# Optimization experiments

Measured on AMD Instinct MI355X. Metric: run time of the kernel, lower is better.

Reference implementation:

```python
import jax, jax.numpy as jnp
import numpy as np

N = 100000   # nodes
E = 1600000  # edges
D = 64       # hidden dim == num_features
L = 3        # num_gc_layers
C = 10       # num_classes
G = 512      # num graphs in batch
BN_EPS = 1e-5


def setup_inputs() -> dict:
    key = jax.random.key(0)
    ks = jax.random.split(key, 12)
    s = 1.0 / np.sqrt(D)
    return {
        "x": jax.random.normal(ks[0], (N, D), dtype=jnp.float32),
        "edge_index": jax.random.randint(ks[1], (2, E), 0, N, dtype=jnp.int64),
        "batch": jnp.sort(jax.random.randint(ks[2], (N,), 0, G, dtype=jnp.int64)),
        # GINConv MLP params (layer 0 input dim == D, so all layers stack)
        "w1": jax.random.normal(ks[3], (L, D, D), dtype=jnp.float32) * s,
        "b1": jnp.zeros((L, D), dtype=jnp.float32),
        "w2": jax.random.normal(ks[4], (L, D, D), dtype=jnp.float32) * s,
        "b2": jnp.zeros((L, D), dtype=jnp.float32),
        # BatchNorm affine params
        "gamma": jnp.ones((L, D), dtype=jnp.float32),
        "beta": jnp.zeros((L, D), dtype=jnp.float32),
        # final MLP
        "lin_w": jax.random.normal(ks[5], (L * D, D), dtype=jnp.float32) / np.sqrt(L * D),
        "lin_b": jnp.zeros((D,), dtype=jnp.float32),
        "fin_w": jax.random.normal(ks[6], (D, C), dtype=jnp.float32) * s,
        "fin_b": jnp.zeros((C,), dtype=jnp.float32),
    }


def reference(x, edge_index, batch, w1, b1, w2, b2, gamma, beta, lin_w, lin_b, fin_w, fin_b):
    src, dst = edge_index[0], edge_index[1]
    pooled = []
    h = x
    for i in range(L):
        # GINConv (eps=0): (1+eps)*h_i + sum_{j->i} h_j, then 2-layer MLP
        agg = h + jax.ops.segment_sum(h[src], dst, num_segments=N)  # [N, D]
        z = jax.nn.relu(agg @ w1[i] + b1[i]) @ w2[i] + b2[i]
        z = jax.nn.relu(z)
        # BatchNorm1d (training-mode batch statistics, biased variance)
        mean = jnp.mean(z, axis=0)
        var = jnp.var(z, axis=0)
        h = (z - mean) * (gamma[i] / jnp.sqrt(var + BN_EPS)) + beta[i]
        # global_add_pool: segment-sum over graph ids
        pooled.append(jax.ops.segment_sum(h, batch, num_segments=G))  # [G, D]
    xp = jnp.concatenate(pooled, axis=1)  # [G, L*D]
    out = jax.nn.relu(xp @ lin_w + lin_b) @ fin_w + fin_b  # [G, C]
    return jax.nn.log_softmax(out, axis=-1)
```

## Files before the change

### kernel.cpp

```cpp
#include <hip/hip_runtime.h>

#define BN_EPS 1e-5f
#define TN 128
#define NPB 256
#define BCAP 8192
#define BH_EPB 8192
#define PT_EPB 4096

typedef __attribute__((ext_vector_type(8))) short bf16x8;
typedef __attribute__((ext_vector_type(4))) float f32x4;

static __device__ __forceinline__ unsigned short f2bf(float f) {
    unsigned u = __float_as_uint(f);
    u += 0x7fff + ((u >> 16) & 1);
    return (unsigned short)(u >> 16);
}
static __device__ __forceinline__ float bf2f(unsigned short s) {
    return __uint_as_float(((unsigned)s) << 16);
}

__global__ __launch_bounds__(256) void xbf_kernel(
    const float* __restrict__ x, unsigned short* __restrict__ xbf, int n4)
{
    const int i = blockIdx.x * 256 + threadIdx.x;
    if (i < n4) {
        const float4 v = reinterpret_cast<const float4*>(x)[i];
        ushort4 o;
        o.x = f2bf(v.x); o.y = f2bf(v.y); o.z = f2bf(v.z); o.w = f2bf(v.w);
        reinterpret_cast<ushort4*>(xbf)[i] = o;
    }
}

__global__ __launch_bounds__(256) void bh_kernel(
    const int* __restrict__ dst, int* __restrict__ bucketCnt, int E, int NB)
{
    __shared__ int lh[512];
    const int tid = threadIdx.x;
    for (int i = tid; i < NB; i += 256) lh[i] = 0;
    __syncthreads();
    const int base = blockIdx.x * BH_EPB;
#pragma unroll
    for (int k = 0; k < BH_EPB / 256; ++k) {
        const int e = base + k * 256 + tid;
        if (e < E) atomicAdd(&lh[dst[e] >> 8], 1);
    }
    __syncthreads();
    for (int i = tid; i < NB; i += 256) {
        const int c = lh[i];
        if (c > 0) atomicAdd(&bucketCnt[i], c);
    }
}

__global__ __launch_bounds__(512) void bscan_kernel(
    const int* __restrict__ bucketCnt, int* __restrict__ bucketStart,
    int* __restrict__ bucketCursor, int NB)
{
    __shared__ int ls[512];
    const int t = threadIdx.x;
    const int v = (t < NB) ? bucketCnt[t] : 0;
    ls[t] = v;
    __syncthreads();
    for (int off = 1; off < 512; off <<= 1) {
        const int a = ls[t];
        const int b = (t >= off) ? ls[t - off] : 0;
        __syncthreads();
        ls[t] = a + b;
        __syncthreads();
    }
    const int excl = ls[t] - v;
    if (t < NB) { bucketStart[t] = excl; bucketCursor[t] = excl; }
    if (t == 511) bucketStart[NB] = ls[511];
}

__global__ __launch_bounds__(256) void part_kernel(
    const int* __restrict__ src, const int* __restrict__ dst,
    int* __restrict__ bucketCursor, unsigned* __restrict__ part, int E, int NB)
{
    __shared__ int lh[512];
    __shared__ int lbase[512];
    const int tid = threadIdx.x;
    const int base = blockIdx.x * PT_EPB;
    for (int i = tid; i < NB; i += 256) lh[i] = 0;
    __syncthreads();
#pragma unroll
    for (int k = 0; k < PT_EPB / 256; ++k) {
        const int e = base + k * 256 + tid;
        if (e < E) atomicAdd(&lh[dst[e] >> 8], 1);
    }
    __syncthreads();
    for (int i = tid; i < NB; i += 256) {
        const int c = lh[i];
        lbase[i] = (c > 0) ? atomicAdd(&bucketCursor[i], c) : 0;
        lh[i] = 0;
    }
    __syncthreads();
#pragma unroll
    for (int k = 0; k < PT_EPB / 256; ++k) {
        const int e = base + k * 256 + tid;
        if (e < E) {
            const int d = dst[e];
            const int b = d >> 8;
            const int off = atomicAdd(&lh[b], 1);
            part[lbase[b] + off] = ((unsigned)src[e] << 8) | (unsigned)(d & 255);
        }
    }
}

__global__ __launch_bounds__(256) void bcsr_kernel(
    const unsigned* __restrict__ part, const int* __restrict__ bucketStart,
    int* __restrict__ deg, int* __restrict__ rowstart,
    int* __restrict__ eidx, int nN)
{
    __shared__ unsigned sSrc[BCAP];
    __shared__ int ldeg[256], ls[256], lcur[256];
    const int b = blockIdx.x;
    const int tid = threadIdx.x;
    const int sStart = bucketStart[b];
    const int cnt = bucketStart[b + 1] - sStart;
    const bool ldsok = (cnt <= BCAP);

    ldeg[tid] = 0;
    __syncthreads();
    for (int i = tid; i < cnt; i += 256) {
        const unsigned v = part[sStart + i];
        if (ldsok) sSrc[i] = v;
        atomicAdd(&ldeg[v & 255u], 1);
    }
    __syncthreads();
    const int dv = ldeg[tid];
    ls[tid] = dv;
    __syncthreads();
    for (int off = 1; off < 256; off <<= 1) {
        const int a = ls[tid];
        const int c = (tid >= off) ? ls[tid - off] : 0;
        __syncthreads();
        ls[tid] = a + c;
        __syncthreads();
    }
    const int excl = ls[tid] - dv;
    lcur[tid] = excl;
    const int node = b * NPB + tid;
    if (node < nN) {
        deg[node] = dv;
        rowstart[node] = sStart + excl;
    }
    __syncthreads();
    for (int i = tid; i < cnt; i += 256) {
        const unsigned v = ldsok ? sSrc[i] : part[sStart + i];
        const int dloc = (int)(v & 255u);
        const int p = atomicAdd(&lcur[dloc], 1);
        eidx[sStart + p] = (int)(v >> 8);
    }
}

__global__ __launch_bounds__(256) void cnt_kernel(
    const int* __restrict__ batch, int* __restrict__ cnt, int nN)
{
    const int n = blockIdx.x * 256 + threadIdx.x;
    if (n >= nN) return;
    const int g = batch[n];
    const bool firstb = (n == 0) || (batch[n - 1] != g);
    const bool lastb  = (n == nN - 1) || (batch[n + 1] != g);
    if (lastb)  atomicAdd(&cnt[g], n + 1);
    if (firstb) atomicAdd(&cnt[g], -n);
}

__global__ __launch_bounds__(256) void agg_kernel(
    const unsigned short* __restrict__ z, const float* __restrict__ scsh,
    const int* __restrict__ rowstart, const int* __restrict__ deg,
    const int* __restrict__ eidx, unsigned short* __restrict__ agg, int nN)
{
    const int node = blockIdx.x * 4 + (threadIdx.x >> 6);
    if (node >= nN) return;
    const int lane = threadIdx.x & 63;
    const int q = lane >> 4;
    const int fr = (lane & 15) * 4;
    const int rs = rowstart[node];
    const int d = deg[node];

    float a0 = 0.f, a1 = 0.f, a2 = 0.f, a3 = 0.f;
    if (q == 0) {
        const ushort4 v = *reinterpret_cast<const ushort4*>(z + (size_t)node * 64 + fr);
        a0 = bf2f(v.x); a1 = bf2f(v.y); a2 = bf2f(v.z); a3 = bf2f(v.w);
    }
    for (int i = 0; i < d; i += 16) {
        const int j0 = i + q, j1 = j0 + 4, j2 = j0 + 8, j3 = j0 + 12;
        const int c0 = min(j0, d - 1), c1 = min(j1, d - 1);
        const int c2 = min(j2, d - 1), c3 = min(j3, d - 1);
        const int s0 = eidx[rs + c0], s1 = eidx[rs + c1];
        const int s2 = eidx[rs + c2], s3 = eidx[rs + c3];
        const ushort4 v0 = *reinterpret_cast<const ushort4*>(z + (size_t)s0 * 64 + fr);
        const ushort4 v1 = *reinterpret_cast<const ushort4*>(z + (size_t)s1 * 64 + fr);
        const ushort4 v2 = *reinterpret_cast<const ushort4*>(z + (size_t)s2 * 64 + fr);
        const ushort4 v3 = *reinterpret_cast<const ushort4*>(z + (size_t)s3 * 64 + fr);
        const float w0 = (j0 < d) ? 1.f : 0.f;
        const float w1 = (j1 < d) ? 1.f : 0.f;
        const float w2 = (j2 < d) ? 1.f : 0.f;
        const float w3 = (j3 < d) ? 1.f : 0.f;
        a0 = fmaf(w0, bf2f(v0.x), a0); a1 = fmaf(w0, bf2f(v0.y), a1);
        a2 = fmaf(w0, bf2f(v0.z), a2); a3 = fmaf(w0, bf2f(v0.w), a3);
        a0 = fmaf(w1, bf2f(v1.x), a0); a1 = fmaf(w1, bf2f(v1.y), a1);
        a2 = fmaf(w1, bf2f(v1.z), a2); a3 = fmaf(w1, bf2f(v1.w), a3);
        a0 = fmaf(w2, bf2f(v2.x), a0); a1 = fmaf(w2, bf2f(v2.y), a1);
        a2 = fmaf(w2, bf2f(v2.z), a2); a3 = fmaf(w2, bf2f(v2.w), a3);
        a0 = fmaf(w3, bf2f(v3.x), a0); a1 = fmaf(w3, bf2f(v3.y), a1);
        a2 = fmaf(w3, bf2f(v3.z), a2); a3 = fmaf(w3, bf2f(v3.w), a3);
    }
    a0 += __shfl_xor(a0, 16); a0 += __shfl_xor(a0, 32);
    a1 += __shfl_xor(a1, 16); a1 += __shfl_xor(a1, 32);
    a2 += __shfl_xor(a2, 16); a2 += __shfl_xor(a2, 32);
    a3 += __shfl_xor(a3, 16); a3 += __shfl_xor(a3, 32);
    if (lane < 16) {
        float4 sc = make_float4(1.f, 1.f, 1.f, 1.f);
        float4 sh = make_float4(0.f, 0.f, 0.f, 0.f);
        if (scsh) {
            sc = *reinterpret_cast<const float4*>(scsh + fr);
            sh = *reinterpret_cast<const float4*>(scsh + 64 + fr);
        }
        const float c = (float)(d + 1);
        ushort4 ob;
        ob.x = f2bf(fmaf(a0, sc.x, c * sh.x));
        ob.y = f2bf(fmaf(a1, sc.y, c * sh.y));
        ob.z = f2bf(fmaf(a2, sc.z, c * sh.z));
        ob.w = f2bf(fmaf(a3, sc.w, c * sh.w));
        *reinterpret_cast<ushort4*>(agg + (size_t)node * 64 + fr) = ob;
    }
}

__global__ __launch_bounds__(256) void mlp_kernel(
    const unsigned short* __restrict__ agg, const int* __restrict__ batch,
    const float* __restrict__ w1, const float* __restrict__ b1,
    const float* __restrict__ w2, const float* __restrict__ b2,
    unsigned short* __restrict__ zout, float* __restrict__ bnstats,
    float* __restrict__ xpz, int layer, int nN)
{
    __shared__ unsigned short sA[128 * 72];
    __shared__ unsigned short sW[2][64 * 72];
    __shared__ float sB[2][64];
    __shared__ float sSum[64], sSq[64];
    __shared__ float sPool[4 * 64];
    __shared__ int sBatch[128];

    const int tid = threadIdx.x;
    const int n0 = blockIdx.x * TN;

    {
        const int row = tid >> 1;
        const int cg = (tid & 1) * 32;
        const int node = n0 + row;
        uint4 v0 = make_uint4(0, 0, 0, 0), v1 = v0, v2 = v0, v3 = v0;
        if (node < nN) {
            const uint4* g = reinterpret_cast<const uint4*>(agg + (size_t)node * 64 + cg);
            v0 = g[0]; v1 = g[1]; v2 = g[2]; v3 = g[3];
        }
        uint4* dp = reinterpret_cast<uint4*>(&sA[row * 72 + cg]);
        dp[0] = v0; dp[1] = v1; dp[2] = v2; dp[3] = v3;
    }
    {
        const int j = tid & 63;
        const int kb = (tid >> 6) * 16;
        const float* ws1 = w1 + (size_t)layer * 4096;
        const float* ws2 = w2 + (size_t)layer * 4096;
#pragma unroll 4
        for (int i = 0; i < 16; ++i) {
            const int k = kb + i;
            sW[0][j * 72 + k] = f2bf(ws1[k * 64 + j]);
            sW[1][j * 72 + k] = f2bf(ws2[k * 64 + j]);
        }
        if (tid < 64) {
            sB[0][tid] = b1[layer * 64 + tid];
            sB[1][tid] = b2[layer * 64 + tid];
            sSum[tid] = 0.f; sSq[tid] = 0.f;
        }
        if (tid < 128) sBatch[tid] = (n0 + tid < nN) ? batch[n0 + tid] : -1;
        sPool[tid] = 0.f;
    }
    __syncthreads();

    const int w  = tid >> 6;
    const int l  = tid & 63;
    const int lr = l & 15;
    const int hi = l >> 4;

    f32x4 acc[2][4];
#pragma unroll
    for (int rt = 0; rt < 2; ++rt)
#pragma unroll
        for (int ct = 0; ct < 4; ++ct) {
            const float bv = sB[0][ct * 16 + lr];
            acc[rt][ct] = (f32x4){bv, bv, bv, bv};
        }
#pragma unroll
    for (int kb = 0; kb < 2; ++kb) {
        const bf16x8 af0 = *reinterpret_cast<const bf16x8*>(&sA[(w * 32 + lr) * 72 + kb * 32 + hi * 8]);
        const bf16x8 af1 = *reinterpret_cast<const bf16x8*>(&sA[(w * 32 + 16 + lr) * 72 + kb * 32 + hi * 8]);
#pragma unroll
        for (int ct = 0; ct < 4; ++ct) {
            const bf16x8 bfr = *reinterpret_cast<const bf16x8*>(&sW[0][(ct * 16 + lr) * 72 + kb * 32 + hi * 8]);
            acc[0][ct] = __builtin_amdgcn_mfma_f32_16x16x32_bf16(af0, bfr, acc[0][ct], 0, 0, 0);
            acc[1][ct] = __builtin_amdgcn_mfma_f32_16x16x32_bf16(af1, bfr, acc[1][ct], 0, 0, 0);
        }
    }
    __syncthreads();
#pragma unroll
    for (int rt = 0; rt < 2; ++rt)
#pragma unroll
        for (int ct = 0; ct < 4; ++ct)
#pragma unroll
            for (int r = 0; r < 4; ++r)
                sA[(w * 32 + rt * 16 + hi * 4 + r) * 72 + ct * 16 + lr] =
                    f2bf(fmaxf(acc[rt][ct][r], 0.f));
    __syncthreads();

#pragma unroll
    for (int rt = 0; rt < 2; ++rt)
#pragma unroll
        for (int ct = 0; ct < 4; ++ct) {
            const float bv = sB[1][ct * 16 + lr];
            acc[rt][ct] = (f32x4){bv, bv, bv, bv};
        }
#pragma unroll
    for (int kb = 0; kb < 2; ++kb) {
        const bf16x8 af0 = *reinterpret_cast<const bf16x8*>(&sA[(w * 32 + lr) * 72 + kb * 32 + hi * 8]);
        const bf16x8 af1 = *reinterpret_cast<const bf16x8*>(&sA[(w * 32 + 16 + lr) * 72 + kb * 32 + hi * 8]);
#pragma unroll
        for (int ct = 0; ct < 4; ++ct) {
            const bf16x8 bfr = *reinterpret_cast<const bf16x8*>(&sW[1][(ct * 16 + lr) * 72 + kb * 32 + hi * 8]);
            acc[0][ct] = __builtin_amdgcn_mfma_f32_16x16x32_bf16(af0, bfr, acc[0][ct], 0, 0, 0);
            acc[1][ct] = __builtin_amdgcn_mfma_f32_16x16x32_bf16(af1, bfr, acc[1][ct], 0, 0, 0);
        }
    }

    const int gfirst = sBatch[0];
#pragma unroll
    for (int rt = 0; rt < 2; ++rt) {
#pragma unroll
        for (int ct = 0; ct < 4; ++ct) {
            const int j = ct * 16 + lr;
            float s = 0.f, q = 0.f;
            int curg = -1;
            float ps = 0.f;
#pragma unroll
            for (int r = 0; r < 4; ++r) {
                const int lrow = w * 32 + rt * 16 + hi * 4 + r;
                const int node = n0 + lrow;
                const float v = fmaxf(acc[rt][ct][r], 0.f);
                if (node < nN) {
                    zout[(size_t)node * 64 + j] = f2bf(v);
                    s += v; q += v * v;
                    const int g = sBatch[lrow];
                    if (g != curg) {
                        if (curg >= 0) {
                            const int lg = curg - gfirst;
                            if (lg < 4) atomicAdd(&sPool[lg * 64 + j], ps);
                            else        atomicAdd(&xpz[(size_t)curg * 64 + j], ps);
                        }
                        curg = g; ps = 0.f;
                    }
                    ps += v;
                }
            }
            if (curg >= 0) {
                const int lg = curg - gfirst;
                if (lg < 4) atomicAdd(&sPool[lg * 64 + j], ps);
                else        atomicAdd(&xpz[(size_t)curg * 64 + j], ps);
            }
            s += __shfl_xor(s, 16); s += __shfl_xor(s, 32);
            q += __shfl_xor(q, 16); q += __shfl_xor(q, 32);
            if (hi == 0) { atomicAdd(&sSum[j], s); atomicAdd(&sSq[j], q); }
        }
    }
    __syncthreads();
    {
        const int lg = tid >> 6, d = tid & 63;
        const float v = sPool[tid];
        if (v != 0.f) atomicAdd(&xpz[(size_t)(gfirst + lg) * 64 + d], v);
    }
    if (tid < 64) {
        atomicAdd(&bnstats[tid], sSum[tid]);
        atomicAdd(&bnstats[64 + tid], sSq[tid]);
    }
}

__global__ __launch_bounds__(256) void finalize_kernel(
    float* __restrict__ xp, const float* __restrict__ bnstats,
    const float* __restrict__ gamma, const float* __restrict__ beta,
    const int* __restrict__ cnt, float* __restrict__ xpz,
    float* __restrict__ scsh, int layer, int nG, float invN)
{
    const int i = blockIdx.x * 256 + threadIdx.x;
    if (i >= nG * 64) return;
    const int g = i >> 6, d = i & 63;
    const float mean = bnstats[d] * invN;
    const float var  = fmaxf(bnstats[64 + d] * invN - mean * mean, 0.f);
    const float sc = gamma[layer * 64 + d] * rsqrtf(var + BN_EPS);
    const float sh = beta[layer * 64 + d] - mean * sc;
    if (g == 0) { scsh[d] = sc; scsh[64 + d] = sh; }
    xp[(size_t)g * 192 + layer * 64 + d] = fmaf(sc, xpz[i], (float)cnt[g] * sh);
    xpz[i] = 0.f;
}

__global__ __launch_bounds__(256) void final_kernel(
    const float* __restrict__ xp, const float* __restrict__ lin_w,
    const float* __restrict__ lin_b, const float* __restrict__ fin_w,
    const float* __restrict__ fin_b, float* __restrict__ out, int nG)
{
    const int g = (blockIdx.x * 256 + threadIdx.x) >> 6;
    const int lane = threadIdx.x & 63;
    if (g >= nG) return;
    const float* xr = xp + (size_t)g * 192;
    float acc = lin_b[lane];
    for (int k = 0; k < 192; ++k) acc = fmaf(xr[k], lin_w[k * 64 + lane], acc);
    const float t = fmaxf(acc, 0.f);
    float o[10];
#pragma unroll
    for (int c = 0; c < 10; ++c) {
        float p = t * fin_w[lane * 10 + c];
#pragma unroll
        for (int off = 32; off > 0; off >>= 1) p += __shfl_xor(p, off);
        o[c] = p + fin_b[c];
    }
    float m = o[0];
#pragma unroll
    for (int c = 1; c < 10; ++c) m = fmaxf(m, o[c]);
    float Z = 0.f;
#pragma unroll
    for (int c = 0; c < 10; ++c) Z += expf(o[c] - m);
    const float lz = m + logf(Z);
#pragma unroll
    for (int c = 0; c < 10; ++c)
        if (lane == c) out[(size_t)g * 10 + c] = o[c] - lz;
}

extern "C" void kernel_launch(void* const* d_in, const int* in_sizes, int n_in,
                              void* d_out, int out_size, void* d_ws, size_t ws_size,
                              hipStream_t stream)
{
    const float* x     = (const float*)d_in[0];
    const int*   ei    = (const int*)d_in[1];
    const int*   batch = (const int*)d_in[2];
    const float* w1    = (const float*)d_in[3];
    const float* b1    = (const float*)d_in[4];
    const float* w2    = (const float*)d_in[5];
    const float* b2    = (const float*)d_in[6];
    const float* gamma = (const float*)d_in[7];
    const float* beta  = (const float*)d_in[8];
    const float* lin_w = (const float*)d_in[9];
    const float* lin_b = (const float*)d_in[10];
    const float* fin_w = (const float*)d_in[11];
    const float* fin_b = (const float*)d_in[12];
    float* out = (float*)d_out;

    const int N = in_sizes[0] / 64;
    const int E = in_sizes[1] / 2;
    const int L = in_sizes[3] / 4096;
    const int G = out_size / 10;
    const float invN = 1.0f / (float)N;
    const int NB = (N + NPB - 1) / NPB;

    char* ws = (char*)d_ws;
    size_t off = 0;
    auto alloc = [&](size_t bytes) -> void* {
        void* p = ws + off;
        off += (bytes + 255) & ~(size_t)255;
        return p;
    };
    unsigned short* xbf = (unsigned short*)alloc((size_t)N * 64 * 2);
    unsigned short* z0  = (unsigned short*)alloc((size_t)N * 64 * 2);
    unsigned short* z1  = (unsigned short*)alloc((size_t)N * 64 * 2);
    unsigned short* aggbuf = (unsigned short*)alloc((size_t)N * 64 * 2);
    float* xp      = (float*)alloc((size_t)G * 192 * 4);
    float* xpz     = (float*)alloc((size_t)G * 64 * 4);
    float* bnstats = (float*)alloc((size_t)L * 128 * 4);
    float* scsh    = (float*)alloc(128 * 4);
    int*   cnt      = (int*)alloc((size_t)G * 4);
    int*   deg      = (int*)alloc((size_t)N * 4);
    int*   rowstart = (int*)alloc((size_t)N * 4);
    int*   eidx     = (int*)alloc((size_t)E * 4);
    unsigned* part  = (unsigned*)alloc((size_t)E * 4);
    int*   bucketCnt    = (int*)alloc((size_t)NB * 4);
    int*   bucketStart  = (int*)alloc((size_t)(NB + 1) * 4);
    int*   bucketCursor = (int*)alloc((size_t)NB * 4);

    const int* srcIdx = ei;
    const int* dstIdx = ei + E;

    hipMemsetAsync(bucketCnt, 0, (size_t)NB * 4, stream);
    hipMemsetAsync(bnstats, 0, (size_t)L * 128 * 4, stream);
    hipMemsetAsync(xpz, 0, (size_t)G * 64 * 4, stream);
    hipMemsetAsync(cnt, 0, (size_t)G * 4, stream);
    bh_kernel<<<(E + BH_EPB - 1) / BH_EPB, 256, 0, stream>>>(dstIdx, bucketCnt, E, NB);
    bscan_kernel<<<1, 512, 0, stream>>>(bucketCnt, bucketStart, bucketCursor, NB);
    part_kernel<<<(E + PT_EPB - 1) / PT_EPB, 256, 0, stream>>>(
        srcIdx, dstIdx, bucketCursor, part, E, NB);
    bcsr_kernel<<<NB, 256, 0, stream>>>(part, bucketStart, deg, rowstart, eidx, N);
    cnt_kernel<<<(N + 255) / 256, 256, 0, stream>>>(batch, cnt, N);
    xbf_kernel<<<(N * 16 + 255) / 256, 256, 0, stream>>>(x, xbf, N * 16);

    const int nAggBlk = (N + 3) / 4;
    const int nMlpBlk = (N + TN - 1) / TN;
    unsigned short* zprev = xbf;
    unsigned short* zcur = z0;
    for (int l = 0; l < L; ++l) {
        agg_kernel<<<nAggBlk, 256, 0, stream>>>(
            zprev, (l == 0) ? nullptr : scsh,
            rowstart, deg, eidx, aggbuf, N);
        mlp_kernel<<<nMlpBlk, 256, 0, stream>>>(
            aggbuf, batch, w1, b1, w2, b2,
            zcur, bnstats + (size_t)l * 128, xpz, l, N);
        finalize_kernel<<<(G * 64 + 255) / 256, 256, 0, stream>>>(
            xp, bnstats + (size_t)l * 128, gamma, beta, cnt, xpz, scsh, l, G, invN);
        zprev = zcur;
        zcur = (zcur == z0) ? z1 : z0;
    }
    final_kernel<<<(G * 64 + 255) / 256, 256, 0, stream>>>(xp, lin_w, lin_b,
                                                           fin_w, fin_b, out, G);
}
```

Measured before the change: 333.0 us.

## Pre-transpose weights to bf16, widen agg gathers, skip last-layer z store

Adds a one-time kernel that transposes and converts w1/w2 to bf16, so each MLP block loads its weights with vectorized copies instead of strided float reads and per-element conversion. The aggregation kernel now has each lane gather 16-byte rows (8 bf16 features) with 8 neighbors per iteration, prefetching the next edge index. The final layer no longer writes z, which nothing downstream reads. The BN-statistics loop is reordered so the shuffle reductions happen once per column tile instead of per row tile. The trade is fewer neighbors in flight per iteration in agg and one extra small launch.

```diff
diff --git a/kernel.cpp b/kernel.cpp
--- a/kernel.cpp
+++ b/kernel.cpp
@@ -29,6 +29,35 @@
         o.x = f2bf(v.x); o.y = f2bf(v.y); o.z = f2bf(v.z); o.w = f2bf(v.w);
         reinterpret_cast<ushort4*>(xbf)[i] = o;
     }
+}
+
+__global__ __launch_bounds__(256) void wtbf_kernel(
+    const float* __restrict__ w1, const float* __restrict__ w2,
+    unsigned short* __restrict__ wtb)
+{
+    __shared__ float sT[64 * 65];
+    const int b = blockIdx.x;
+    const int t = threadIdx.x;
+    const float* src = ((b & 1) ? w2 : w1) + (size_t)(b >> 1) * 4096;
+#pragma unroll
+    for (int rr = 0; rr < 4; ++rr) {
+        const int i = (rr * 256 + t) * 4;
+        const float4 v = *reinterpret_cast<const float4*>(src + i);
+        const int k = i >> 6, j = i & 63;
+        sT[(j + 0) * 65 + k] = v.x;
+        sT[(j + 1) * 65 + k] = v.y;
+        sT[(j + 2) * 65 + k] = v.z;
+        sT[(j + 3) * 65 + k] = v.w;
+    }
+    __syncthreads();
+    const int j = t >> 2;
+    const int kb = (t & 3) * 16;
+    unsigned short o[16];
+#pragma unroll
+    for (int i = 0; i < 16; ++i) o[i] = f2bf(sT[j * 65 + kb + i]);
+    uint4* dp = reinterpret_cast<uint4*>(wtb + ((size_t)b * 64 + j) * 64 + kb);
+    dp[0] = *reinterpret_cast<const uint4*>(&o[0]);
+    dp[1] = *reinterpret_cast<const uint4*>(&o[8]);
 }
 
 __global__ __launch_bounds__(256) void bh_kernel(
@@ -173,66 +202,58 @@
     const int node = blockIdx.x * 4 + (threadIdx.x >> 6);
     if (node >= nN) return;
     const int lane = threadIdx.x & 63;
-    const int q = lane >> 4;
-    const int fr = (lane & 15) * 4;
+    const int q = lane >> 3;
+    const int fe = (lane & 7) * 8;
     const int rs = rowstart[node];
     const int d = deg[node];
 
-    float a0 = 0.f, a1 = 0.f, a2 = 0.f, a3 = 0.f;
+    float a[8] = {0.f, 0.f, 0.f, 0.f, 0.f, 0.f, 0.f, 0.f};
     if (q == 0) {
-        const ushort4 v = *reinterpret_cast<const ushort4*>(z + (size_t)node * 64 + fr);
-        a0 = bf2f(v.x); a1 = bf2f(v.y); a2 = bf2f(v.z); a3 = bf2f(v.w);
-    }
-    for (int i = 0; i < d; i += 16) {
-        const int j0 = i + q, j1 = j0 + 4, j2 = j0 + 8, j3 = j0 + 12;
-        const int c0 = min(j0, d - 1), c1 = min(j1, d - 1);
-        const int c2 = min(j2, d - 1), c3 = min(j3, d - 1);
-        const int s0 = eidx[rs + c0], s1 = eidx[rs + c1];
-        const int s2 = eidx[rs + c2], s3 = eidx[rs + c3];
-        const ushort4 v0 = *reinterpret_cast<const ushort4*>(z + (size_t)s0 * 64 + fr);
-        const ushort4 v1 = *reinterpret_cast<const ushort4*>(z + (size_t)s1 * 64 + fr);
-        const ushort4 v2 = *reinterpret_cast<const ushort4*>(z + (size_t)s2 * 64 + fr);
-        const ushort4 v3 = *reinterpret_cast<const ushort4*>(z + (size_t)s3 * 64 + fr);
-        const float w0 = (j0 < d) ? 1.f : 0.f;
-        const float w1 = (j1 < d) ? 1.f : 0.f;
-        const float w2 = (j2 < d) ? 1.f : 0.f;
-        const float w3 = (j3 < d) ? 1.f : 0.f;
-        a0 = fmaf(w0, bf2f(v0.x), a0); a1 = fmaf(w0, bf2f(v0.y), a1);
-        a2 = fmaf(w0, bf2f(v0.z), a2); a3 = fmaf(w0, bf2f(v0.w), a3);
-        a0 = fmaf(w1, bf2f(v1.x), a0); a1 = fmaf(w1, bf2f(v1.y), a1);
-        a2 = fmaf(w1, bf2f(v1.z), a2); a3 = fmaf(w1, bf2f(v1.w), a3);
-        a0 = fmaf(w2, bf2f(v2.x), a0); a1 = fmaf(w2, bf2f(v2.y), a1);
-        a2 = fmaf(w2, bf2f(v2.z), a2); a3 = fmaf(w2, bf2f(v2.w), a3);
-        a0 = fmaf(w3, bf2f(v3.x), a0); a1 = fmaf(w3, bf2f(v3.y), a1);
-        a2 = fmaf(w3, bf2f(v3.z), a2); a3 = fmaf(w3, bf2f(v3.w), a3);
-    }
-    a0 += __shfl_xor(a0, 16); a0 += __shfl_xor(a0, 32);
-    a1 += __shfl_xor(a1, 16); a1 += __shfl_xor(a1, 32);
-    a2 += __shfl_xor(a2, 16); a2 += __shfl_xor(a2, 32);
-    a3 += __shfl_xor(a3, 16); a3 += __shfl_xor(a3, 32);
-    if (lane < 16) {
-        float4 sc = make_float4(1.f, 1.f, 1.f, 1.f);
-        float4 sh = make_float4(0.f, 0.f, 0.f, 0.f);
+        const uint4 v = *reinterpret_cast<const uint4*>(z + (size_t)node * 64 + fe);
+        const unsigned short* e = reinterpret_cast<const unsigned short*>(&v);
+#pragma unroll
+        for (int k = 0; k < 8; ++k) a[k] = bf2f(e[k]);
+    }
+    if (d > 0) {
+        int s = eidx[rs + min(q, d - 1)];
+        for (int i = 0; i < d; i += 8) {
+            const int j = i + q;
+            const float w = (j < d) ? 1.f : 0.f;
+            const uint4 v = *reinterpret_cast<const uint4*>(z + (size_t)s * 64 + fe);
+            s = eidx[rs + min(i + 8 + q, d - 1)];
+            const unsigned short* e = reinterpret_cast<const unsigned short*>(&v);
+#pragma unroll
+            for (int k = 0; k < 8; ++k) a[k] = fmaf(w, bf2f(e[k]), a[k]);
+        }
+    }
+#pragma unroll
+    for (int k = 0; k < 8; ++k) {
+        a[k] += __shfl_xor(a[k], 8);
+        a[k] += __shfl_xor(a[k], 16);
+        a[k] += __shfl_xor(a[k], 32);
+    }
+    if (q == 0) {
+        unsigned short ob[8];
         if (scsh) {
-            sc = *reinterpret_cast<const float4*>(scsh + fr);
-            sh = *reinterpret_cast<const float4*>(scsh + 64 + fr);
-        }
-        const float c = (float)(d + 1);
-        ushort4 ob;
-        ob.x = f2bf(fmaf(a0, sc.x, c * sh.x));
-        ob.y = f2bf(fmaf(a1, sc.y, c * sh.y));
-        ob.z = f2bf(fmaf(a2, sc.z, c * sh.z));
-        ob.w = f2bf(fmaf(a3, sc.w, c * sh.w));
-        *reinterpret_cast<ushort4*>(agg + (size_t)node * 64 + fr) = ob;
+            const float c = (float)(d + 1);
+#pragma unroll
+            for (int k = 0; k < 8; ++k)
+                ob[k] = f2bf(fmaf(a[k], scsh[fe + k], c * scsh[64 + fe + k]));
+        } else {
+#pragma unroll
+            for (int k = 0; k < 8; ++k) ob[k] = f2bf(a[k]);
+        }
+        *reinterpret_cast<uint4*>(agg + (size_t)node * 64 + fe) =
+            *reinterpret_cast<const uint4*>(&ob[0]);
     }
 }
 
 __global__ __launch_bounds__(256) void mlp_kernel(
     const unsigned short* __restrict__ agg, const int* __restrict__ batch,
-    const float* __restrict__ w1, const float* __restrict__ b1,
-    const float* __restrict__ w2, const float* __restrict__ b2,
+    const unsigned short* __restrict__ wtb, const float* __restrict__ b1,
+    const float* __restrict__ b2,
     unsigned short* __restrict__ zout, float* __restrict__ bnstats,
-    float* __restrict__ xpz, int layer, int nN)
+    float* __restrict__ xpz, int layer, int nN, int storeZ)
 {
     __shared__ unsigned short sA[128 * 72];
     __shared__ unsigned short sW[2][64 * 72];
@@ -257,16 +278,13 @@
         dp[0] = v0; dp[1] = v1; dp[2] = v2; dp[3] = v3;
     }
     {
-        const int j = tid & 63;
-        const int kb = (tid >> 6) * 16;
-        const float* ws1 = w1 + (size_t)layer * 4096;
-        const float* ws2 = w2 + (size_t)layer * 4096;
-#pragma unroll 4
-        for (int i = 0; i < 16; ++i) {
-            const int k = kb + i;
-            sW[0][j * 72 + k] = f2bf(ws1[k * 64 + j]);
-            sW[1][j * 72 + k] = f2bf(ws2[k * 64 + j]);
-        }
+        const int m = tid >> 7;
+        const int j = (tid & 127) >> 1;
+        const int cg = (tid & 1) * 32;
+        const uint4* g = reinterpret_cast<const uint4*>(
+            wtb + (((size_t)layer * 2 + m) * 64 + j) * 64 + cg);
+        uint4* dp = reinterpret_cast<uint4*>(&sW[m][j * 72 + cg]);
+        dp[0] = g[0]; dp[1] = g[1]; dp[2] = g[2]; dp[3] = g[3];
         if (tid < 64) {
             sB[0][tid] = b1[layer * 64 + tid];
             sB[1][tid] = b2[layer * 64 + tid];
@@ -333,11 +351,11 @@
 
     const int gfirst = sBatch[0];
 #pragma unroll
-    for (int rt = 0; rt < 2; ++rt) {
-#pragma unroll
-        for (int ct = 0; ct < 4; ++ct) {
-            const int j = ct * 16 + lr;
-            float s = 0.f, q = 0.f;
+    for (int ct = 0; ct < 4; ++ct) {
+        const int j = ct * 16 + lr;
+        float s = 0.f, qsum = 0.f;
+#pragma unroll
+        for (int rt = 0; rt < 2; ++rt) {
             int curg = -1;
             float ps = 0.f;
 #pragma unroll
@@ -346,8 +364,8 @@
                 const int node = n0 + lrow;
                 const float v = fmaxf(acc[rt][ct][r], 0.f);
                 if (node < nN) {
-                    zout[(size_t)node * 64 + j] = f2bf(v);
-                    s += v; q += v * v;
+                    if (storeZ) zout[(size_t)node * 64 + j] = f2bf(v);
+                    s += v; qsum += v * v;
                     const int g = sBatch[lrow];
                     if (g != curg) {
                         if (curg >= 0) {
@@ -365,10 +383,10 @@
                 if (lg < 4) atomicAdd(&sPool[lg * 64 + j], ps);
                 else        atomicAdd(&xpz[(size_t)curg * 64 + j], ps);
             }
-            s += __shfl_xor(s, 16); s += __shfl_xor(s, 32);
-            q += __shfl_xor(q, 16); q += __shfl_xor(q, 32);
-            if (hi == 0) { atomicAdd(&sSum[j], s); atomicAdd(&sSq[j], q); }
-        }
+        }
+        s += __shfl_xor(s, 16); s += __shfl_xor(s, 32);
+        qsum += __shfl_xor(qsum, 16); qsum += __shfl_xor(qsum, 32);
+        if (hi == 0) { atomicAdd(&sSum[j], s); atomicAdd(&sSq[j], qsum); }
     }
     __syncthreads();
     {
@@ -469,6 +487,7 @@
     unsigned short* z0  = (unsigned short*)alloc((size_t)N * 64 * 2);
     unsigned short* z1  = (unsigned short*)alloc((size_t)N * 64 * 2);
     unsigned short* aggbuf = (unsigned short*)alloc((size_t)N * 64 * 2);
+    unsigned short* wtb = (unsigned short*)alloc((size_t)L * 2 * 4096 * 2);
     float* xp      = (float*)alloc((size_t)G * 192 * 4);
     float* xpz     = (float*)alloc((size_t)G * 64 * 4);
     float* bnstats = (float*)alloc((size_t)L * 128 * 4);
@@ -496,6 +515,7 @@
     bcsr_kernel<<<NB, 256, 0, stream>>>(part, bucketStart, deg, rowstart, eidx, N);
     cnt_kernel<<<(N + 255) / 256, 256, 0, stream>>>(batch, cnt, N);
     xbf_kernel<<<(N * 16 + 255) / 256, 256, 0, stream>>>(x, xbf, N * 16);
+    wtbf_kernel<<<L * 2, 256, 0, stream>>>(w1, w2, wtb);
 
     const int nAggBlk = (N + 3) / 4;
     const int nMlpBlk = (N + TN - 1) / TN;
@@ -506,8 +526,8 @@
             zprev, (l == 0) ? nullptr : scsh,
             rowstart, deg, eidx, aggbuf, N);
         mlp_kernel<<<nMlpBlk, 256, 0, stream>>>(
-            aggbuf, batch, w1, b1, w2, b2,
-            zcur, bnstats + (size_t)l * 128, xpz, l, N);
+            aggbuf, batch, wtb, b1, b2,
+            zcur, bnstats + (size_t)l * 128, xpz, l, N, (l < L - 1) ? 1 : 0);
         finalize_kernel<<<(G * 64 + 255) / 256, 256, 0, stream>>>(
             xp, bnstats + (size_t)l * 128, gamma, beta, cnt, xpz, scsh, l, G, invN);
         zprev = zcur;
```

Result: slower. 342.5 us (+2.8%).
